# Optimization experiments

Hardware: AMD Instinct MI355X
Metric: run time of the kernel (lower is better)

Reference implementation:

```python
import jax, jax.numpy as jnp
import numpy as np

B, DIM, H, W = 64, 384, 28, 28
NH, HD, WS, SS = 6, 64, 7, 3
HID = 1536
N = WS * WS
NW = (H // WS) * (W // WS)
SCALE = HD ** -0.25  # qk_scale=None -> head_dim ** -0.25, applied to both q and k
EPS = 1e-5


def _rel_pos_index(ws):
    coords = np.stack(np.meshgrid(np.arange(ws), np.arange(ws), indexing='ij'))  # (2,ws,ws)
    flat = coords.reshape(2, -1)
    rel = (flat[:, :, None] - flat[:, None, :]).transpose(1, 2, 0).copy()  # (N,N,2)
    rel[..., 0] += ws - 1
    rel[..., 1] += ws - 1
    rel[..., 0] *= 2 * ws - 1
    return rel.sum(-1)  # (N,N) int


def _attn_mask(h, w, ws, ss):
    img = np.zeros((h, w))
    cnt = 0
    for hs in (slice(0, -ws), slice(-ws, -ss), slice(-ss, None)):
        for wsl in (slice(0, -ws), slice(-ws, -ss), slice(-ss, None)):
            img[hs, wsl] = cnt
            cnt += 1
    mw = img.reshape(h // ws, ws, w // ws, ws).transpose(0, 2, 1, 3).reshape(-1, ws * ws)  # (nW,N)
    diff = mw[:, None, :] - mw[:, :, None]
    return np.where(diff != 0, -100.0, 0.0).astype(np.float32)  # (nW,N,N)


REL_IDX = jnp.asarray(_rel_pos_index(WS))          # (N,N)
MASK = jnp.asarray(_attn_mask(H, W, WS, SS))       # (NW,N,N)


def _layernorm_bchw(x, w, b):
    mean = jnp.mean(x, axis=1, keepdims=True)
    var = jnp.var(x, axis=1, keepdims=True, ddof=1)  # torch.var_mean is unbiased
    return (x - mean) / jnp.sqrt(var + EPS) * w + b


def setup_inputs() -> dict:
    key = jax.random.key(0)
    ks = jax.random.split(key, 6)
    return {
        'x': jax.random.normal(ks[0], (B, DIM, H, W), jnp.float32),
        'norm1_w': jnp.ones((1, DIM, 1, 1), jnp.float32),
        'norm1_b': jnp.zeros((1, DIM, 1, 1), jnp.float32),
        'qkv_w': jax.random.normal(ks[1], (3 * NH * HD, DIM), jnp.float32) * 0.02,
        'rel_bias_table': jax.random.normal(ks[2], ((2 * WS - 1) ** 2, NH), jnp.float32) * 0.02,
        'proj_w': jax.random.normal(ks[3], (DIM, NH * HD), jnp.float32) * 0.02,
        'norm2_w': jnp.ones((1, DIM, 1, 1), jnp.float32),
        'norm2_b': jnp.zeros((1, DIM, 1, 1), jnp.float32),
        'mlp_w1': jax.random.normal(ks[4], (HID, DIM), jnp.float32) * 0.02,
        'mlp_w3': jax.random.normal(ks[5], (DIM, HID), jnp.float32) * 0.02,
    }


def reference(x, norm1_w, norm1_b, qkv_w, rel_bias_table, proj_w, norm2_w, norm2_b, mlp_w1, mlp_w3):
    b = x.shape[0]
    shortcut = x
    xn = _layernorm_bchw(x, norm1_w, norm1_b)
    xs = jnp.roll(xn, (-SS, -SS), axis=(2, 3))
    # window partition: (B,C,H,W) -> (B*nW, C, WS, WS)
    xw = xs.reshape(b, DIM, H // WS, WS, W // WS, WS).transpose(0, 2, 4, 1, 3, 5).reshape(-1, DIM, WS, WS)
    bw = xw.shape[0]
    # 1x1-conv qkv projection (no bias), then split heads
    qkv = jnp.einsum('oc,bchw->bohw', qkv_w, xw).reshape(bw, 3, NH, HD, N)
    q, k, v = jnp.moveaxis(qkv, 1, 0)  # each (bw, NH, HD, N)
    attn = jnp.einsum('bhdn,bhdm->bhnm', q * SCALE, k * SCALE)  # (bw,NH,N,N)
    bias = rel_bias_table[REL_IDX.reshape(-1)].reshape(N, N, NH).transpose(2, 0, 1)  # (NH,N,N)
    attn = attn + bias[None]
    attn = attn.reshape(b, NW, NH, N, N) + MASK[None, :, None]
    attn = jax.nn.softmax(attn.reshape(bw, NH, N, N), axis=-1)
    out = jnp.einsum('bhnm,bhdm->bhdn', attn, v)  # (bw,NH,HD,N)
    out = out.reshape(bw, NH * HD, WS, WS)
    out = jnp.einsum('oc,bchw->bohw', proj_w, out)
    # window reverse + unshift
    xr = out.reshape(b, H // WS, W // WS, DIM, WS, WS).transpose(0, 3, 1, 4, 2, 5).reshape(b, DIM, H, W)
    xr = jnp.roll(xr, (SS, SS), axis=(2, 3))
    x = shortcut + xr
    # conv MLP (1x1 convs, no bias, exact GELU)
    xn2 = _layernorm_bchw(x, norm2_w, norm2_b)
    h = jax.nn.gelu(jnp.einsum('oc,bchw->bohw', mlp_w1, xn2), approximate=False)
    x = x + jnp.einsum('oc,bchw->bohw', mlp_w3, h)
    return x
```

## Files before the change

### kernel.cpp

```cpp
#include <hip/hip_runtime.h>
#include <hip/hip_bf16.h>


typedef __bf16 bf16x8 __attribute__((ext_vector_type(8)));
typedef __bf16 bf16x4 __attribute__((ext_vector_type(4)));
typedef float  f32x4  __attribute__((ext_vector_type(4)));
typedef int    i32x4  __attribute__((ext_vector_type(4)));

#define GAS __attribute__((address_space(1)))
#define LAS __attribute__((address_space(3)))

__device__ __forceinline__ int div7u(int m) { return (m * 37) >> 8; }

__device__ __forceinline__ float gelu_f(float v) {
  float s = fabsf(v) * 0.70710678118f;
  float t = __builtin_amdgcn_rcpf(__builtin_fmaf(0.3275911f, s, 1.f));
  float p = t * (0.254829592f +
            t * (-0.284496736f +
            t * (1.421413741f +
            t * (-1.453152027f +
            t * 1.061405429f))));
  float erfa = __builtin_fmaf(-p, __expf(-s * s), 1.f);
  return __builtin_fmaf(0.5f * fabsf(v), erfa, 0.5f * v);
}

__global__ __launch_bounds__(256) void cvt_all_kernel(const float* __restrict__ s0,
                                                      const float* __restrict__ s1,
                                                      const float* __restrict__ s2,
                                                      const float* __restrict__ s3,
                                                      __bf16* __restrict__ d0,
                                                      __bf16* __restrict__ d1,
                                                      __bf16* __restrict__ d2,
                                                      __bf16* __restrict__ d3) {
  int i = blockIdx.x * 256 + threadIdx.x;
  if (i < 442368) { d0[i] = (__bf16)s0[i]; return; }
  i -= 442368;
  if (i < 147456) { d1[i] = (__bf16)s1[i]; return; }
  i -= 147456;
  if (i < 589824) { d2[i] = (__bf16)s2[i]; return; }
  i -= 589824;
  d3[i] = (__bf16)s3[i];
}

__global__ __launch_bounds__(256) void bias_expand_kernel(const float* __restrict__ tbl,
                                                          float* __restrict__ be) {
  int idx = blockIdx.x * 256 + threadIdx.x;
  if (idx >= 6 * 64 * 64) return;
  int m = idx & 63, n = (idx >> 6) & 63, h = idx >> 12;
  float v = 0.f;
  if (m < 49 && n < 49) {
    int in_ = div7u(n), jn = n - in_ * 7;
    int im  = div7u(m), jm = m - im * 7;
    int t = (in_ - im + 6) * 13 + (jn - jm + 6);
    v = tbl[t * 6 + h];
  }
  be[idx] = v;
}

__global__ __launch_bounds__(256) void ln_t_kernel(const float* __restrict__ x,
                                                   const float* __restrict__ gw,
                                                   const float* __restrict__ gb,
                                                   __bf16* __restrict__ out) {
  __shared__ f32x4 ps[16][16], ps2[16][16];
  __shared__ __align__(16) __bf16 tile[64][198];
  const int tid = threadIdx.x;
  const int lane = tid & 63, w = tid >> 6;
  const int gq = lane & 15;
  const int sub = (w << 2) + (lane >> 4);
  const int tok0 = blockIdx.x << 6;
  const int tokg4 = tok0 + (gq << 2);
  const unsigned b = (unsigned)tokg4 / 784u;
  const unsigned p = (unsigned)tokg4 - b * 784u;
  const float* xp = x + (size_t)b * 301056u + p;

  f32x4 vals[24];
  f32x4 s4 = {0.f, 0.f, 0.f, 0.f}, s24 = {0.f, 0.f, 0.f, 0.f};
  #pragma unroll
  for (int half = 0; half < 2; ++half)
    #pragma unroll
    for (int k = 0; k < 12; ++k) {
      int c = half * 192 + sub * 12 + k;
      f32x4 v = *(const f32x4*)(xp + (size_t)c * 784u);
      vals[half * 12 + k] = v;
      s4 += v;
      s24 += v * v;
    }
  ps[sub][gq] = s4;
  ps2[sub][gq] = s24;
  __syncthreads();
  f32x4 S = {0.f, 0.f, 0.f, 0.f}, S2 = {0.f, 0.f, 0.f, 0.f};
  #pragma unroll
  for (int i = 0; i < 16; ++i) { S += ps[i][gq]; S2 += ps2[i][gq]; }
  f32x4 mean = S * (1.f / 384.f);
  f32x4 var = (S2 - S * mean) * (1.f / 383.f);
  f32x4 rstd;
  #pragma unroll
  for (int j = 0; j < 4; ++j) rstd[j] = rsqrtf(var[j] + 1e-5f);

  #pragma unroll
  for (int half = 0; half < 2; ++half) {
    if (half) __syncthreads();
    #pragma unroll
    for (int k = 0; k < 12; ++k) {
      int c = half * 192 + sub * 12 + k;
      float wgt = gw[c], bia = gb[c];
      f32x4 v = (vals[half * 12 + k] - mean) * rstd * wgt + bia;
      #pragma unroll
      for (int j = 0; j < 4; ++j)
        tile[(gq << 2) + j][sub * 12 + k] = (__bf16)v[j];
    }
    __syncthreads();
    #pragma unroll
    for (int it = 0; it < 6; ++it) {
      int idx = (it << 8) + tid;
      int row = idx / 24, colc = idx - row * 24;
      bf16x8 vv = *(const bf16x8*)(&tile[row][colc << 3]);
      *(bf16x8*)(out + (size_t)(tok0 + row) * 384 + half * 192 + (colc << 3)) = vv;
    }
  }
}

template <int EPI>
__global__ __launch_bounds__(256, 3) void gemm_bt(const __bf16* __restrict__ A, int lda,
                                                  const __bf16* __restrict__ Bt, int ldb,
                                                  int K, int My,
                                                  __bf16* __restrict__ outT, int ldo, int ocol,
                                                  float* __restrict__ outR,
                                                  const float* __restrict__ resid,
                                                  int tok_off) {
  __shared__ __align__(16) char smem[33792];
  const int tid = threadIdx.x;
  const int lane = tid & 63;
  const int w = tid >> 6;
  const int wr = w >> 1, wc = w & 1;
  const int c = lane & 15, g = lane >> 4;

  const int nwg = gridDim.x;
  const int orig = blockIdx.x;
  const int q = nwg >> 3, r = nwg & 7;
  const int xcd = orig & 7, ii = orig >> 3;
  const int wgid = (xcd < r ? xcd * (q + 1) : r * (q + 1) + (xcd - r) * q) + ii;
  const int bx = wgid / My;
  const int by = wgid - bx * My;
  const int m0 = by << 7;
  const int n0 = bx << 7;

  const __bf16* ap[4];
  const __bf16* bp[4];
  #pragma unroll
  for (int i = 0; i < 4; ++i) {
    int s = (i << 8) + tid;
    int row = s >> 3;
    int kk = ((s ^ row) & 7) << 3;
    ap[i] = A  + (size_t)(m0 + row) * lda + kk;
    bp[i] = Bt + (size_t)(n0 + row) * ldb + kk;
  }

  i32x4 sA0, sA1, sA2, sA3, sB0, sB1, sB2, sB3;
  auto issue = [&](int k0) {
    sA0 = *(const i32x4*)(ap[0] + k0); sB0 = *(const i32x4*)(bp[0] + k0);
    sA1 = *(const i32x4*)(ap[1] + k0); sB1 = *(const i32x4*)(bp[1] + k0);
    sA2 = *(const i32x4*)(ap[2] + k0); sB2 = *(const i32x4*)(bp[2] + k0);
    sA3 = *(const i32x4*)(ap[3] + k0); sB3 = *(const i32x4*)(bp[3] + k0);
  };
  auto write_lds = [&]() {
    *(i32x4*)(smem +         (((0 << 8) + tid) << 4)) = sA0;
    *(i32x4*)(smem +         (((1 << 8) + tid) << 4)) = sA1;
    *(i32x4*)(smem +         (((2 << 8) + tid) << 4)) = sA2;
    *(i32x4*)(smem +         (((3 << 8) + tid) << 4)) = sA3;
    *(i32x4*)(smem + 16384 + (((0 << 8) + tid) << 4)) = sB0;
    *(i32x4*)(smem + 16384 + (((1 << 8) + tid) << 4)) = sB1;
    *(i32x4*)(smem + 16384 + (((2 << 8) + tid) << 4)) = sB2;
    *(i32x4*)(smem + 16384 + (((3 << 8) + tid) << 4)) = sB3;
  };

  f32x4 acc[4][4] = {};
  const int nt = K >> 6;

  issue(0);
  write_lds();
  asm volatile("s_waitcnt lgkmcnt(0)" ::: "memory");
  __builtin_amdgcn_s_barrier();
  __builtin_amdgcn_sched_barrier(0);

  for (int t = 0; t < nt; ++t) {
    if (t + 1 < nt) issue((t + 1) << 6);
    const char* smA = smem;
    const char* smB = smem + 16384;
    #pragma unroll
    for (int ks = 0; ks < 2; ++ks) {
      bf16x8 af[4], bfv[4];
      #pragma unroll
      for (int mi = 0; mi < 4; ++mi) {
        int r2 = (wr << 6) + (mi << 4) + c;
        af[mi] = *(const bf16x8*)(smA + (r2 << 7) + (((ks << 6) + (g << 4)) ^ ((r2 & 7) << 4)));
      }
      #pragma unroll
      for (int nj = 0; nj < 4; ++nj) {
        int r2 = (wc << 6) + (nj << 4) + c;
        bfv[nj] = *(const bf16x8*)(smB + (r2 << 7) + (((ks << 6) + (g << 4)) ^ ((r2 & 7) << 4)));
      }
      #pragma unroll
      for (int mi = 0; mi < 4; ++mi)
        #pragma unroll
        for (int nj = 0; nj < 4; ++nj) {
          if constexpr (EPI == 2)
            acc[mi][nj] = __builtin_amdgcn_mfma_f32_16x16x32_bf16(bfv[nj], af[mi], acc[mi][nj], 0, 0, 0);
          else
            acc[mi][nj] = __builtin_amdgcn_mfma_f32_16x16x32_bf16(af[mi], bfv[nj], acc[mi][nj], 0, 0, 0);
        }
    }
    __builtin_amdgcn_s_barrier();
    if (t + 1 < nt) {
      write_lds();
      asm volatile("s_waitcnt lgkmcnt(0)" ::: "memory");
    }
    __builtin_amdgcn_s_barrier();
    __builtin_amdgcn_sched_barrier(0);
  }

  if constexpr (EPI <= 1) {
    #pragma unroll
    for (int mi = 0; mi < 4; ++mi)
      #pragma unroll
      for (int nj = 0; nj < 4; ++nj) {
        f32x4 v = acc[mi][nj];
        if constexpr (EPI == 1) {
          #pragma unroll
          for (int r2 = 0; r2 < 4; ++r2) v[r2] = gelu_f(v[r2]);
        }
        bf16x4 pk = {(__bf16)v[0], (__bf16)v[1], (__bf16)v[2], (__bf16)v[3]};
        int nl = (wc << 6) + (nj << 4) + c;
        int ml = (wr << 6) + (mi << 4) + (g << 2);
        *(bf16x4*)(smem + nl * 264 + ml * 2) = pk;
      }
    __syncthreads();
    #pragma unroll
    for (int it = 0; it < 8; ++it) {
      int id = (it << 8) + tid;
      int n = id >> 4, mc = id & 15;
      bf16x8 v = *(const bf16x8*)(smem + n * 264 + (mc << 4));
      *(bf16x8*)(outT + (size_t)(n0 + n) * ldo + (ocol + m0 + (mc << 3))) = v;
    }
  } else {
    #pragma unroll
    for (int nj = 0; nj < 4; ++nj) {
      int tokb = tok_off + n0 + (wc << 6) + (nj << 4) + (g << 2);
      unsigned bb = (unsigned)tokb / 784u;
      unsigned pp = (unsigned)tokb - bb * 784u;
      size_t base2 = (size_t)bb * (384u * 784u) + pp;
      #pragma unroll
      for (int mi = 0; mi < 4; ++mi) {
        int o = m0 + (wr << 6) + (mi << 4) + c;
        size_t a2 = base2 + (size_t)o * 784u;
        f32x4 rv = *(const f32x4*)(resid + a2);
        f32x4 v = acc[mi][nj] + rv;
        *(f32x4*)(outR + a2) = v;
      }
    }
  }
}

__global__ __launch_bounds__(256, 2) void attn_kernel(const __bf16* __restrict__ qkv,
                                                      const float* __restrict__ be,
                                                      __bf16* __restrict__ outt) {
  __shared__ __align__(16) char smem_all[4][16384];
  const int tid = threadIdx.x;
  const int lane = tid & 63;
  const int w = tid >> 6;
  char* sm = (char*)smem_all[w];
  const int pair = blockIdx.x * 4 + w;
  const int h = pair % 6;
  const int wg = pair / 6;
  const int b = wg >> 4;
  const int wi = wg & 15;
  const int wh = wi >> 2, wwi = wi & 3;
  const int cc = lane & 15, g = lane >> 4;

  {
    int rsub = lane >> 3;
    int slot = lane & 7;
    int dc = (slot ^ rsub) << 3;
    #pragma unroll
    for (int i = 0; i < 8; ++i) {
      int r = i * 8 + rsub;
      int m = r < 49 ? r : 48;
      int im = div7u(m), jm = m - im * 7;
      int sh = wh * 7 + im + 3; if (sh >= 28) sh -= 28;
      int sw = wwi * 7 + jm + 3; if (sw >= 28) sw -= 28;
      size_t trow = (size_t)(b * 784 + sh * 28 + sw) * 1152;
      __builtin_amdgcn_global_load_lds((const GAS void*)(qkv + trow + 384 + h * 64 + dc),
                                       (LAS void*)(sm + i * 1024), 16, 0, 0);
      __builtin_amdgcn_global_load_lds((const GAS void*)(qkv + trow + h * 64 + dc),
                                       (LAS void*)(sm + 8192 + i * 1024), 16, 0, 0);
    }
  }
  asm volatile("s_waitcnt vmcnt(0)" ::: "memory");
  __syncthreads();

  f32x4 sacc[4][4] = {};
  #pragma unroll
  for (int ks = 0; ks < 2; ++ks) {
    bf16x8 kf[4], qf[4];
    #pragma unroll
    for (int mi = 0; mi < 4; ++mi) {
      int r = (mi << 4) + cc;
      kf[mi] = *(const bf16x8*)(sm + (r << 7) + (((ks << 6) + (g << 4)) ^ ((r & 7) << 4)));
    }
    #pragma unroll
    for (int nj = 0; nj < 4; ++nj) {
      int r = (nj << 4) + cc;
      qf[nj] = *(const bf16x8*)(sm + 8192 + (r << 7) + (((ks << 6) + (g << 4)) ^ ((r & 7) << 4)));
    }
    #pragma unroll
    for (int mi = 0; mi < 4; ++mi)
      #pragma unroll
      for (int nj = 0; nj < 4; ++nj)
        sacc[mi][nj] = __builtin_amdgcn_mfma_f32_16x16x32_bf16(kf[mi], qf[nj], sacc[mi][nj], 0, 0, 0);
  }
  __syncthreads();

  int r9m[4][4];
  #pragma unroll
  for (int mi = 0; mi < 4; ++mi)
    #pragma unroll
    for (int rr = 0; rr < 4; ++rr) {
      int m = (mi << 4) + (g << 2) + rr; if (m > 48) m = 48;
      int im = div7u(m), jm = m - im * 7;
      int sh = wh * 7 + im, sw = wwi * 7 + jm;
      r9m[mi][rr] = ((sh < 21) ? 0 : (sh < 25 ? 1 : 2)) * 3 + ((sw < 21) ? 0 : (sw < 25 ? 1 : 2));
    }

  #pragma unroll
  for (int nj = 0; nj < 4; ++nj) {
    int n = (nj << 4) + cc;
    int ncl = n > 48 ? 48 : n;
    int in_ = div7u(ncl), jn = ncl - in_ * 7;
    int shn = wh * 7 + in_, swn = wwi * 7 + jn;
    int r9n = ((shn < 21) ? 0 : (shn < 25 ? 1 : 2)) * 3 + ((swn < 21) ? 0 : (swn < 25 ? 1 : 2));
    float mx = -1e30f;
    #pragma unroll
    for (int mi = 0; mi < 4; ++mi) {
      f32x4 bia = *(const f32x4*)(be + (((h << 6) + n) << 6) + (mi << 4) + (g << 2));
      #pragma unroll
      for (int rr = 0; rr < 4; ++rr) {
        int m = (mi << 4) + (g << 2) + rr;
        float t = (m < 49)
            ? sacc[mi][nj][rr] * 0.125f + bia[rr] + ((r9m[mi][rr] == r9n) ? 0.f : -100.f)
            : -1e30f;
        sacc[mi][nj][rr] = t;
        mx = fmaxf(mx, t);
      }
    }
    mx = fmaxf(mx, __shfl_xor(mx, 16, 64));
    mx = fmaxf(mx, __shfl_xor(mx, 32, 64));
    float sum = 0.f;
    #pragma unroll
    for (int mi = 0; mi < 4; ++mi)
      #pragma unroll
      for (int rr = 0; rr < 4; ++rr) {
        float e = __expf(sacc[mi][nj][rr] - mx);
        sacc[mi][nj][rr] = e;
        sum += e;
      }
    sum += __shfl_xor(sum, 16, 64);
    sum += __shfl_xor(sum, 32, 64);
    float inv = __builtin_amdgcn_rcpf(sum);
    #pragma unroll
    for (int mi = 0; mi < 4; ++mi) {
      bf16x4 pk = {(__bf16)(sacc[mi][nj][0] * inv), (__bf16)(sacc[mi][nj][1] * inv),
                   (__bf16)(sacc[mi][nj][2] * inv), (__bf16)(sacc[mi][nj][3] * inv)};
      *(bf16x4*)(sm + 8192 + (n << 7) + (((mi << 5) + (g << 3)) ^ ((n & 7) << 4))) = pk;
    }
  }

  {
    int ml = lane & 15, dq = lane >> 4;
    #pragma unroll
    for (int it = 0; it < 4; ++it) {
      int m = (it << 4) + ml;
      int mc_ = m > 48 ? 48 : m;
      int im = div7u(mc_), jm = mc_ - im * 7;
      int sh = wh * 7 + im + 3; if (sh >= 28) sh -= 28;
      int sw = wwi * 7 + jm + 3; if (sw >= 28) sw -= 28;
      const __bf16* gv = qkv + (size_t)(b * 784 + sh * 28 + sw) * 1152 + 768 + h * 64;
      #pragma unroll
      for (int hd = 0; hd < 2; ++hd) {
        int dbase = (hd << 5) + (dq << 3);
        bf16x8 v = *(const bf16x8*)(gv + dbase);
        #pragma unroll
        for (int j = 0; j < 8; ++j) {
          int d = dbase + j;
          *(__bf16*)(sm + (d << 7) + ((((m >> 3) ^ (d & 7)) << 4) + ((m & 7) << 1))) = v[j];
        }
      }
    }
  }
  __syncthreads();

  f32x4 oacc[4][4] = {};
  #pragma unroll
  for (int ks = 0; ks < 2; ++ks) {
    bf16x8 pf[4], vf[4];
    #pragma unroll
    for (int ni = 0; ni < 4; ++ni) {
      int n = (ni << 4) + cc;
      pf[ni] = *(const bf16x8*)(sm + 8192 + (n << 7) + (((ks << 6) + (g << 4)) ^ ((n & 7) << 4)));
    }
    #pragma unroll
    for (int dj = 0; dj < 4; ++dj) {
      int d = (dj << 4) + cc;
      vf[dj] = *(const bf16x8*)(sm + (d << 7) + ((((ks << 2) + g) ^ (d & 7)) << 4));
    }
    #pragma unroll
    for (int ni = 0; ni < 4; ++ni)
      #pragma unroll
      for (int dj = 0; dj < 4; ++dj)
        oacc[ni][dj] = __builtin_amdgcn_mfma_f32_16x16x32_bf16(pf[ni], vf[dj], oacc[ni][dj], 0, 0, 0);
  }

  #pragma unroll
  for (int ni = 0; ni < 4; ++ni)
    #pragma unroll
    for (int rr = 0; rr < 4; ++rr) {
      int n = (ni << 4) + (g << 2) + rr;
      if (n < 49) {
        int im = div7u(n), jn = n - im * 7;
        int sh = wh * 7 + im + 3; if (sh >= 28) sh -= 28;
        int sw = wwi * 7 + jn + 3; if (sw >= 28) sw -= 28;
        __bf16* op = outt + (size_t)(b * 784 + sh * 28 + sw) * 384 + h * 64;
        #pragma unroll
        for (int dj = 0; dj < 4; ++dj)
          op[(dj << 4) + cc] = (__bf16)oacc[ni][dj][rr];
      }
    }
}

extern "C" void kernel_launch(void* const* d_in, const int* in_sizes, int n_in,
                              void* d_out, int out_size, void* d_ws, size_t ws_size,
                              hipStream_t stream) {
  (void)in_sizes; (void)n_in; (void)out_size; (void)ws_size;
  const float* x     = (const float*)d_in[0];
  const float* n1w   = (const float*)d_in[1];
  const float* n1b   = (const float*)d_in[2];
  const float* qkvw  = (const float*)d_in[3];
  const float* tbl   = (const float*)d_in[4];
  const float* projw = (const float*)d_in[5];
  const float* n2w   = (const float*)d_in[6];
  const float* n2b   = (const float*)d_in[7];
  const float* w1    = (const float*)d_in[8];
  const float* w3    = (const float*)d_in[9];
  float* out = (float*)d_out;

  char* ws = (char*)d_ws;
  __bf16* bufA = (__bf16*)ws;
  __bf16* bufB = (__bf16*)(ws + 38535168);
  float*  be   = (float*)(ws + 154140672);
  __bf16* wq   = (__bf16*)(ws + 154238976);
  __bf16* wp   = wq + 442368;
  __bf16* wm1  = wp + 147456;
  __bf16* wm3  = wm1 + 589824;

  cvt_all_kernel<<<6912, 256, 0, stream>>>(qkvw, projw, w1, w3, wq, wp, wm1, wm3);
  bias_expand_kernel<<<96, 256, 0, stream>>>(tbl, be);

  ln_t_kernel<<<784, 256, 0, stream>>>(x, n1w, n1b, bufA);
  gemm_bt<0><<<392 * 9, 256, 0, stream>>>(wq, 384, bufA, 384, 384, 9, bufB, 1152, 0,
                                          nullptr, nullptr, 0);
  attn_kernel<<<1536, 256, 0, stream>>>(bufB, be, bufA);
  gemm_bt<2><<<392 * 3, 256, 0, stream>>>(wp, 384, bufA, 384, 384, 3, nullptr, 0, 0,
                                          out, x, 0);
  ln_t_kernel<<<784, 256, 0, stream>>>(out, n2w, n2b, bufA);
  for (int hh = 0; hh < 2; ++hh) {
    const int toff = hh * 25088;
    gemm_bt<1><<<196 * 12, 256, 0, stream>>>(wm1, 384, bufA + (size_t)toff * 384, 384, 384, 12,
                                             bufB, 1536, 0, nullptr, nullptr, 0);
    gemm_bt<2><<<196 * 3, 256, 0, stream>>>(wm3, 1536, bufB, 1536, 1536, 3,
                                            nullptr, 0, 0, out, out, toff);
  }
}
```

Baseline: 401.1 us.

## Store MLP hidden activations in FP8 and switch GELU to tanh approximation

```diff
diff --git a/kernel.cpp b/kernel.cpp
--- a/kernel.cpp
+++ b/kernel.cpp
@@ -5,23 +5,76 @@
 typedef __bf16 bf16x8 __attribute__((ext_vector_type(8)));
 typedef __bf16 bf16x4 __attribute__((ext_vector_type(4)));
 typedef float  f32x4  __attribute__((ext_vector_type(4)));
+typedef float  f32x2  __attribute__((ext_vector_type(2)));
 typedef int    i32x4  __attribute__((ext_vector_type(4)));
+typedef int    i32x2  __attribute__((ext_vector_type(2)));
 
 #define GAS __attribute__((address_space(1)))
 #define LAS __attribute__((address_space(3)))
 
+#if __has_builtin(__builtin_amdgcn_cvt_pk_f32_fp8) && __has_builtin(__builtin_amdgcn_cvt_pk_fp8_f32)
+#define HAS_HW_FP8 1
+#else
+#define HAS_HW_FP8 0
+#endif
+
 __device__ __forceinline__ int div7u(int m) { return (m * 37) >> 8; }
 
+#if !HAS_HW_FP8
+__device__ __forceinline__ float fp8_dec1(unsigned u) {
+  unsigned s = (u >> 7) & 1, e = (u >> 3) & 15, m = u & 7;
+  float nrm = __uint_as_float((s << 31) | ((e + 120) << 23) | (m << 20));
+  float sub = (s ? -1.f : 1.f) * (float)m * 0.001953125f;
+  return e ? nrm : sub;
+}
+__device__ __forceinline__ unsigned fp8_enc1(float f) {
+  f = fminf(fmaxf(f, -448.f), 448.f);
+  unsigned u = __float_as_uint(f);
+  unsigned s = u >> 31;
+  int e8 = (int)((u >> 23) & 255) - 120;
+  unsigned m32 = u & 0x7fffff;
+  if (e8 <= 0) return s << 7;
+  unsigned m = m32 >> 20;
+  unsigned rem = m32 & 0xfffff;
+  m += (rem > 0x80000u) || (rem == 0x80000u && (m & 1));
+  if (m == 8) { m = 0; ++e8; }
+  if (e8 > 15 || (e8 == 15 && m == 7)) { e8 = 15; m = 6; }
+  return (s << 7) | ((unsigned)e8 << 3) | m;
+}
+#endif
+
+template <bool HI>
+__device__ __forceinline__ f32x2 fp8_cvt2(int w) {
+#if HAS_HW_FP8
+  return __builtin_amdgcn_cvt_pk_f32_fp8(w, HI);
+#else
+  unsigned b0 = (w >> (HI ? 16 : 0)) & 255, b1 = (w >> (HI ? 24 : 8)) & 255;
+  return (f32x2){fp8_dec1(b0), fp8_dec1(b1)};
+#endif
+}
+template <bool HI>
+__device__ __forceinline__ int fp8_pk2(float a, float b, int old) {
+#if HAS_HW_FP8
+  return __builtin_amdgcn_cvt_pk_fp8_f32(a, b, old, HI);
+#else
+  unsigned v = fp8_enc1(a) | (fp8_enc1(b) << 8);
+  return HI ? (int)(((unsigned)old & 0xffffu) | (v << 16))
+            : (int)(((unsigned)old & 0xffff0000u) | v);
+#endif
+}
+__device__ __forceinline__ i32x4 fp8x8_to_bf16x8(i32x2 v) {
+  f32x2 a = fp8_cvt2<false>(v[0]), b = fp8_cvt2<true>(v[0]);
+  f32x2 c = fp8_cvt2<false>(v[1]), d = fp8_cvt2<true>(v[1]);
+  bf16x8 r = {(__bf16)a[0], (__bf16)a[1], (__bf16)b[0], (__bf16)b[1],
+              (__bf16)c[0], (__bf16)c[1], (__bf16)d[0], (__bf16)d[1]};
+  return __builtin_bit_cast(i32x4, r);
+}
+
 __device__ __forceinline__ float gelu_f(float v) {
-  float s = fabsf(v) * 0.70710678118f;
-  float t = __builtin_amdgcn_rcpf(__builtin_fmaf(0.3275911f, s, 1.f));
-  float p = t * (0.254829592f +
-            t * (-0.284496736f +
-            t * (1.421413741f +
-            t * (-1.453152027f +
-            t * 1.061405429f))));
-  float erfa = __builtin_fmaf(-p, __expf(-s * s), 1.f);
-  return __builtin_fmaf(0.5f * fabsf(v), erfa, 0.5f * v);
+  float u = v * __builtin_fmaf(0.0356774f, v * v, 0.79788456f);
+  float e = __expf(2.f * u);
+  float t = 1.f - 2.f * __builtin_amdgcn_rcpf(e + 1.f);
+  return 0.5f * v * (1.f + t);
 }
 
 __global__ __launch_bounds__(256) void cvt_all_kernel(const float* __restrict__ s0,
@@ -31,7 +84,9 @@
                                                       __bf16* __restrict__ d0,
                                                       __bf16* __restrict__ d1,
                                                       __bf16* __restrict__ d2,
-                                                      __bf16* __restrict__ d3) {
+                                                      __bf16* __restrict__ d3,
+                                                      const float* __restrict__ tbl,
+                                                      float* __restrict__ be) {
   int i = blockIdx.x * 256 + threadIdx.x;
   if (i < 442368) { d0[i] = (__bf16)s0[i]; return; }
   i -= 442368;
@@ -39,22 +94,18 @@
   i -= 147456;
   if (i < 589824) { d2[i] = (__bf16)s2[i]; return; }
   i -= 589824;
-  d3[i] = (__bf16)s3[i];
-}
-
-__global__ __launch_bounds__(256) void bias_expand_kernel(const float* __restrict__ tbl,
-                                                          float* __restrict__ be) {
-  int idx = blockIdx.x * 256 + threadIdx.x;
-  if (idx >= 6 * 64 * 64) return;
-  int m = idx & 63, n = (idx >> 6) & 63, h = idx >> 12;
-  float v = 0.f;
-  if (m < 49 && n < 49) {
-    int in_ = div7u(n), jn = n - in_ * 7;
-    int im  = div7u(m), jm = m - im * 7;
-    int t = (in_ - im + 6) * 13 + (jn - jm + 6);
-    v = tbl[t * 6 + h];
-  }
-  be[idx] = v;
+  if (i < 589824) { d3[i] = (__bf16)s3[i]; return; }
+  i -= 589824;
+  if (i < 6 * 64 * 64) {
+    int m = i & 63, n = (i >> 6) & 63, h = i >> 12;
+    float v = 0.f;
+    if (m < 49 && n < 49) {
+      int in_ = div7u(n), jn = n - in_ * 7;
+      int im  = div7u(m), jm = m - im * 7;
+      v = tbl[((in_ - im + 6) * 13 + (jn - jm + 6)) * 6 + h];
+    }
+    be[i] = v;
+  }
 }
 
 __global__ __launch_bounds__(256) void ln_t_kernel(const float* __restrict__ x,
@@ -120,14 +171,16 @@
   }
 }
 
-template <int EPI>
+template <int EPI, int F8>
 __global__ __launch_bounds__(256, 3) void gemm_bt(const __bf16* __restrict__ A, int lda,
-                                                  const __bf16* __restrict__ Bt, int ldb,
+                                                  const void* __restrict__ BtV, int ldb,
                                                   int K, int My,
-                                                  __bf16* __restrict__ outT, int ldo, int ocol,
+                                                  void* __restrict__ outT, int ldo, int ocol,
                                                   float* __restrict__ outR,
                                                   const float* __restrict__ resid,
                                                   int tok_off) {
+  constexpr bool B8 = (F8 && EPI == 2);
+  constexpr int esz = B8 ? 1 : 2;
   __shared__ __align__(16) char smem[33792];
   const int tid = threadIdx.x;
   const int lane = tid & 63;
@@ -146,32 +199,52 @@
   const int n0 = bx << 7;
 
   const __bf16* ap[4];
-  const __bf16* bp[4];
+  const unsigned char* bp[4];
   #pragma unroll
   for (int i = 0; i < 4; ++i) {
     int s = (i << 8) + tid;
     int row = s >> 3;
     int kk = ((s ^ row) & 7) << 3;
-    ap[i] = A  + (size_t)(m0 + row) * lda + kk;
-    bp[i] = Bt + (size_t)(n0 + row) * ldb + kk;
-  }
-
-  i32x4 sA0, sA1, sA2, sA3, sB0, sB1, sB2, sB3;
+    ap[i] = A + (size_t)(m0 + row) * lda + kk;
+    bp[i] = (const unsigned char*)BtV + ((size_t)(n0 + row) * ldb + kk) * esz;
+  }
+
+  i32x4 sA0, sA1, sA2, sA3;
+  i32x4 sB0, sB1, sB2, sB3;
+  i32x2 t0, t1, t2, t3;
   auto issue = [&](int k0) {
-    sA0 = *(const i32x4*)(ap[0] + k0); sB0 = *(const i32x4*)(bp[0] + k0);
-    sA1 = *(const i32x4*)(ap[1] + k0); sB1 = *(const i32x4*)(bp[1] + k0);
-    sA2 = *(const i32x4*)(ap[2] + k0); sB2 = *(const i32x4*)(bp[2] + k0);
-    sA3 = *(const i32x4*)(ap[3] + k0); sB3 = *(const i32x4*)(bp[3] + k0);
+    sA0 = *(const i32x4*)(ap[0] + k0);
+    sA1 = *(const i32x4*)(ap[1] + k0);
+    sA2 = *(const i32x4*)(ap[2] + k0);
+    sA3 = *(const i32x4*)(ap[3] + k0);
+    if constexpr (B8) {
+      t0 = *(const i32x2*)(bp[0] + k0);
+      t1 = *(const i32x2*)(bp[1] + k0);
+      t2 = *(const i32x2*)(bp[2] + k0);
+      t3 = *(const i32x2*)(bp[3] + k0);
+    } else {
+      sB0 = *(const i32x4*)(bp[0] + k0 * 2);
+      sB1 = *(const i32x4*)(bp[1] + k0 * 2);
+      sB2 = *(const i32x4*)(bp[2] + k0 * 2);
+      sB3 = *(const i32x4*)(bp[3] + k0 * 2);
+    }
   };
   auto write_lds = [&]() {
     *(i32x4*)(smem +         (((0 << 8) + tid) << 4)) = sA0;
     *(i32x4*)(smem +         (((1 << 8) + tid) << 4)) = sA1;
     *(i32x4*)(smem +         (((2 << 8) + tid) << 4)) = sA2;
     *(i32x4*)(smem +         (((3 << 8) + tid) << 4)) = sA3;
-    *(i32x4*)(smem + 16384 + (((0 << 8) + tid) << 4)) = sB0;
-    *(i32x4*)(smem + 16384 + (((1 << 8) + tid) << 4)) = sB1;
-    *(i32x4*)(smem + 16384 + (((2 << 8) + tid) << 4)) = sB2;
-    *(i32x4*)(smem + 16384 + (((3 << 8) + tid) << 4)) = sB3;
+    if constexpr (B8) {
+      *(i32x4*)(smem + 16384 + (((0 << 8) + tid) << 4)) = fp8x8_to_bf16x8(t0);
+      *(i32x4*)(smem + 16384 + (((1 << 8) + tid) << 4)) = fp8x8_to_bf16x8(t1);
+      *(i32x4*)(smem + 16384 + (((2 << 8) + tid) << 4)) = fp8x8_to_bf16x8(t2);
+      *(i32x4*)(smem + 16384 + (((3 << 8) + tid) << 4)) = fp8x8_to_bf16x8(t3);
+    } else {
+      *(i32x4*)(smem + 16384 + (((0 << 8) + tid) << 4)) = sB0;
+      *(i32x4*)(smem + 16384 + (((1 << 8) + tid) << 4)) = sB1;
+      *(i32x4*)(smem + 16384 + (((2 << 8) + tid) << 4)) = sB2;
+      *(i32x4*)(smem + 16384 + (((3 << 8) + tid) << 4)) = sB3;
+    }
   };
 
   f32x4 acc[4][4] = {};
@@ -240,7 +313,17 @@
       int id = (it << 8) + tid;
       int n = id >> 4, mc = id & 15;
       bf16x8 v = *(const bf16x8*)(smem + n * 264 + (mc << 4));
-      *(bf16x8*)(outT + (size_t)(n0 + n) * ldo + (ocol + m0 + (mc << 3))) = v;
+      if constexpr (F8) {
+        int w0 = 0, w1 = 0;
+        w0 = fp8_pk2<false>((float)v[0], (float)v[1], w0);
+        w0 = fp8_pk2<true>((float)v[2], (float)v[3], w0);
+        w1 = fp8_pk2<false>((float)v[4], (float)v[5], w1);
+        w1 = fp8_pk2<true>((float)v[6], (float)v[7], w1);
+        *(i32x2*)((unsigned char*)outT + (size_t)(n0 + n) * ldo + (ocol + m0 + (mc << 3))) =
+            (i32x2){w0, w1};
+      } else {
+        *(bf16x8*)((__bf16*)outT + (size_t)(n0 + n) * ldo + (ocol + m0 + (mc << 3))) = v;
+      }
     }
   } else {
     #pragma unroll
@@ -461,21 +544,21 @@
   __bf16* wm1  = wp + 147456;
   __bf16* wm3  = wm1 + 589824;
 
-  cvt_all_kernel<<<6912, 256, 0, stream>>>(qkvw, projw, w1, w3, wq, wp, wm1, wm3);
-  bias_expand_kernel<<<96, 256, 0, stream>>>(tbl, be);
+  cvt_all_kernel<<<7008, 256, 0, stream>>>(qkvw, projw, w1, w3, wq, wp, wm1, wm3, tbl, be);
 
   ln_t_kernel<<<784, 256, 0, stream>>>(x, n1w, n1b, bufA);
-  gemm_bt<0><<<392 * 9, 256, 0, stream>>>(wq, 384, bufA, 384, 384, 9, bufB, 1152, 0,
-                                          nullptr, nullptr, 0);
+  gemm_bt<0, 0><<<392 * 9, 256, 0, stream>>>(wq, 384, bufA, 384, 384, 9,
+                                             bufB, 1152, 0, nullptr, nullptr, 0);
   attn_kernel<<<1536, 256, 0, stream>>>(bufB, be, bufA);
-  gemm_bt<2><<<392 * 3, 256, 0, stream>>>(wp, 384, bufA, 384, 384, 3, nullptr, 0, 0,
-                                          out, x, 0);
+  gemm_bt<2, 0><<<392 * 3, 256, 0, stream>>>(wp, 384, bufA, 384, 384, 3,
+                                             nullptr, 0, 0, out, x, 0);
   ln_t_kernel<<<784, 256, 0, stream>>>(out, n2w, n2b, bufA);
+  unsigned char* h8 = (unsigned char*)bufB;
   for (int hh = 0; hh < 2; ++hh) {
     const int toff = hh * 25088;
-    gemm_bt<1><<<196 * 12, 256, 0, stream>>>(wm1, 384, bufA + (size_t)toff * 384, 384, 384, 12,
-                                             bufB, 1536, 0, nullptr, nullptr, 0);
-    gemm_bt<2><<<196 * 3, 256, 0, stream>>>(wm3, 1536, bufB, 1536, 1536, 3,
-                                            nullptr, 0, 0, out, out, toff);
-  }
-}
+    gemm_bt<1, 1><<<196 * 12, 256, 0, stream>>>(wm1, 384, bufA + (size_t)toff * 384, 384, 384, 12,
+                                                (void*)h8, 1536, 0, nullptr, nullptr, 0);
+    gemm_bt<2, 1><<<196 * 3, 256, 0, stream>>>(wm3, 1536, (const void*)h8, 1536, 1536, 3,
+                                               nullptr, 0, 0, out, out, toff);
+  }
+}
```

Result: faster. 392.5 us (-2.2%).
